# Kernel optimization log

Hardware: AMD Instinct MI355X
Metric: run time of the kernel (lower is better)

## Reference

```python
import jax, jax.numpy as jnp
import numpy as np

T, B, N_IN, N_H = 1024, 64, 128, 512

def setup_inputs() -> dict:
    key = jax.random.key(0)
    k1, k2, k3 = jax.random.split(key, 3)
    x = jax.random.normal(k1, (T, B, N_IN), dtype=jnp.float32)
    h0 = jax.random.normal(k2, (B, N_H), dtype=jnp.float32)
    # scale recurrent weights ~ 1/sqrt(fan_in) so tanh does not saturate
    w_rec = jax.random.normal(k3, (N_H, N_H + N_IN + 1), dtype=jnp.float32) * (1.0 / np.sqrt(N_H + N_IN + 1))
    return {"x": x, "h0": h0, "w_rec": w_rec}

def reference(x, h0, w_rec):
    # Elman RNN: h_t = tanh(w_rec @ [h_{t-1}; x_t; 1])
    # x: [T, B, n_in], h0: [B, n_h], w_rec: [n_h, n_h + n_in + 1]
    n_h = h0.shape[-1]
    w_h = w_rec[:, :n_h]            # [n_h, n_h]
    w_x = w_rec[:, n_h:-1]          # [n_h, n_in]
    b = w_rec[:, -1]                # [n_h]
    # precompute input projections for all steps: [T, B, n_h]
    xin = jnp.einsum('tbi,hi->tbh', x, w_x) + b
    def step(h, u):
        h_new = jnp.tanh(jnp.einsum('bk,hk->bh', h, w_h) + u)
        return h_new, h_new
    _, hs = jax.lax.scan(step, h0, xin)
    return hs  # [T, B, n_h]
```

## Files before the change

### kernel.cpp

```cpp
#include <hip/hip_runtime.h>


typedef _Float16 h2 __attribute__((ext_vector_type(2)));

#define T_STEPS 1024
#define B_SZ    64
#define NIN     128
#define NH      512
#define WCOLS   641

__device__ __forceinline__ float fdot2_(h2 a, h2 b, float c) {
#if __has_builtin(__builtin_amdgcn_fdot2)
    return __builtin_amdgcn_fdot2(a, b, c, false);
#else
    return c + (float)a.x * (float)b.x + (float)a.y * (float)b.y;
#endif
}

__device__ __forceinline__ float dot8(uint4 wu, uint4 hu, float acc) {
    union { uint4 u; h2 h[4]; } w, hv;
    w.u = wu; hv.u = hu;
    acc = fdot2_(w.h[0], hv.h[0], acc);
    acc = fdot2_(w.h[1], hv.h[1], acc);
    acc = fdot2_(w.h[2], hv.h[2], acc);
    acc = fdot2_(w.h[3], hv.h[3], acc);
    return acc;
}

__device__ __forceinline__ float fast_tanh(float x) {
    float z = x * 2.8853900817779268f;
#if __has_builtin(__builtin_amdgcn_exp2f)
    float e = __builtin_amdgcn_exp2f(z);
#else
    float e = exp2f(z);
#endif
#if __has_builtin(__builtin_amdgcn_rcpf)
    return 1.f - 2.f * __builtin_amdgcn_rcpf(e + 1.f);
#else
    return 1.f - 2.f / (e + 1.f);
#endif
}

template<int CTRL>
__device__ __forceinline__ float dpp_add(float x) {
    int y = __builtin_amdgcn_update_dpp(0, __builtin_bit_cast(int, x),
                                        CTRL, 0xF, 0xF, true);
    return x + __builtin_bit_cast(float, y);
}

__global__ void prep_kernel(const float* __restrict__ w_rec,
                            float* __restrict__ wxT,
                            float* __restrict__ bias,
                            uint4* __restrict__ Whpk) {
    int g = blockIdx.x * 256 + threadIdx.x;
    if (g < NIN * NH) {
        int i = g >> 9, h = g & (NH - 1);
        wxT[g] = w_rec[h * WCOLS + NH + i];
    } else if (g < NIN * NH + 64 * NH) {
        int m   = g - NIN * NH;
        int c   = m >> 9, tid = m & 511;
        int w   = tid >> 6, lane = tid & 63;
        int rl  = lane >> 3, kl = lane & 7;
        int i   = c & 7, j = c >> 3;
        int row = w * 64 + i * 8 + rl;
        int kg  = kl * 8 + j;
        union { uint4 u; _Float16 f[8]; } pk;
#pragma unroll
        for (int e = 0; e < 8; ++e)
            pk.f[e] = (_Float16)w_rec[row * WCOLS + kg * 8 + e];
        Whpk[c * 512 + tid] = pk.u;
    } else if (g < NIN * NH + 64 * NH + NH) {
        int h = g - (NIN * NH + 64 * NH);
        bias[h] = w_rec[h * WCOLS + NH + NIN];
    }
}

__global__ __launch_bounds__(256) void xin_gemm(const float* __restrict__ x,
                                                const float* __restrict__ wxT,
                                                const float* __restrict__ bias,
                                                float* __restrict__ out) {
    __shared__ float4 xl[128 * 8];
    __shared__ float4 wl[32 * 32];
    __shared__ float  bs[128];
    const int tid = threadIdx.x;
    const int tb0 = blockIdx.x * 128;
    const int hc0 = blockIdx.y * 128;
    if (tid < 128) bs[tid] = bias[hc0 + tid];
    const int tx = tid & 15, ty = tid >> 4;

    float acc[8][8];
#pragma unroll
    for (int r = 0; r < 8; ++r)
#pragma unroll
        for (int c = 0; c < 8; ++c) acc[r][c] = 0.f;

    for (int kc = 0; kc < 4; ++kc) {
        __syncthreads();
#pragma unroll
        for (int l = 0; l < 4; ++l) {
            int idx = tid + 256 * l;
            int row = idx >> 3, c4 = idx & 7;
            xl[idx] = *(const float4*)(x + (long)(tb0 + row) * NIN + kc * 32 + c4 * 4);
        }
#pragma unroll
        for (int l = 0; l < 4; ++l) {
            int idx = tid + 256 * l;
            int ii = idx >> 5, c4 = idx & 31;
            wl[idx] = *(const float4*)(wxT + (kc * 32 + ii) * NH + hc0 + c4 * 4);
        }
        __syncthreads();
#pragma unroll
        for (int i4 = 0; i4 < 8; ++i4) {
            float4 xv[8];
#pragma unroll
            for (int rr = 0; rr < 8; ++rr) xv[rr] = xl[(ty * 8 + rr) * 8 + i4];
#pragma unroll
            for (int j = 0; j < 4; ++j) {
                float4 w0 = wl[(i4 * 4 + j) * 32 + tx * 2];
                float4 w1 = wl[(i4 * 4 + j) * 32 + tx * 2 + 1];
#pragma unroll
                for (int rr = 0; rr < 8; ++rr) {
                    float xs = (j == 0) ? xv[rr].x : (j == 1) ? xv[rr].y
                             : (j == 2) ? xv[rr].z : xv[rr].w;
                    acc[rr][0] += xs * w0.x; acc[rr][1] += xs * w0.y;
                    acc[rr][2] += xs * w0.z; acc[rr][3] += xs * w0.w;
                    acc[rr][4] += xs * w1.x; acc[rr][5] += xs * w1.y;
                    acc[rr][6] += xs * w1.z; acc[rr][7] += xs * w1.w;
                }
            }
        }
    }
#pragma unroll
    for (int rr = 0; rr < 8; ++rr) {
        long row = tb0 + ty * 8 + rr;
        float4 o0, o1;
        o0.x = acc[rr][0] + bs[tx * 8 + 0]; o0.y = acc[rr][1] + bs[tx * 8 + 1];
        o0.z = acc[rr][2] + bs[tx * 8 + 2]; o0.w = acc[rr][3] + bs[tx * 8 + 3];
        o1.x = acc[rr][4] + bs[tx * 8 + 4]; o1.y = acc[rr][5] + bs[tx * 8 + 5];
        o1.z = acc[rr][6] + bs[tx * 8 + 6]; o1.w = acc[rr][7] + bs[tx * 8 + 7];
        *(float4*)(out + row * NH + hc0 + tx * 8)     = o0;
        *(float4*)(out + row * NH + hc0 + tx * 8 + 4) = o1;
    }
}

__global__ __launch_bounds__(512, 2) void rnn_scan(float* __restrict__ out,
                                                   const float* __restrict__ h0,
                                                   const uint4* __restrict__ Whpk) {
    __shared__ uint4 Wl[16 * 512];
    __shared__ uint4 hh[2][72];

    const int tid  = threadIdx.x;
    const int b    = blockIdx.x;
    const int w    = tid >> 6;
    const int lane = tid & 63;
    const int rl   = lane >> 3;
    const int kl   = lane & 7;

#pragma unroll
    for (int c = 0; c < 16; ++c) Wl[c * 512 + tid] = Whpk[(32 + c) * 512 + tid];

    uint4 Wreg[32];
#pragma unroll
    for (int c = 0; c < 32; ++c) Wreg[c] = Whpk[c * 512 + tid];

    {
        int g = tid >> 3, e = tid & 7;
        _Float16* p = (_Float16*)&hh[0][g + (g >> 3)];
        p[e] = (_Float16)h0[b * NH + tid];
    }
    __syncthreads();

    const int own = w * 64 + kl * 8 + rl;
    float* pu = out + (long)b * NH + own;
    float u_cur = *pu;

    for (int t = 0; t < T_STEPS; ++t) {
        const uint4* hc = hh[t & 1];
        uint4 bufA[4], bufB[4];

#pragma unroll
        for (int i = 0; i < 4; ++i) bufA[i] = Whpk[(48 + i) * 512 + tid];
        long stride = (t + 1 < T_STEPS) ? (long)B_SZ * NH : 0;
        float u_nxt = pu[stride];
#pragma unroll
        for (int i = 0; i < 4; ++i) bufB[i] = Whpk[(52 + i) * 512 + tid];

        uint4 hs[8];
#pragma unroll
        for (int j = 0; j < 8; ++j) hs[j] = hc[9 * kl + j];

        float acc[8];
#pragma unroll
        for (int i = 0; i < 8; ++i) acc[i] = 0.f;

#pragma unroll
        for (int j = 0; j < 4; ++j)
#pragma unroll
            for (int i = 0; i < 8; ++i)
                acc[i] = dot8(Wreg[j * 8 + i], hs[j], acc[i]);

#pragma unroll
        for (int i = 0; i < 4; ++i) acc[i] = dot8(bufA[i], hs[6], acc[i]);
#pragma unroll
        for (int i = 0; i < 4; ++i) bufA[i] = Whpk[(56 + i) * 512 + tid];

#pragma unroll
        for (int i = 0; i < 4; ++i) acc[4 + i] = dot8(bufB[i], hs[6], acc[4 + i]);
#pragma unroll
        for (int i = 0; i < 4; ++i) bufB[i] = Whpk[(60 + i) * 512 + tid];

#pragma unroll
        for (int j = 0; j < 2; ++j)
#pragma unroll
            for (int i = 0; i < 8; ++i)
                acc[i] = dot8(Wl[(j * 8 + i) * 512 + tid], hs[4 + j], acc[i]);

#pragma unroll
        for (int i = 0; i < 4; ++i) acc[i] = dot8(bufA[i], hs[7], acc[i]);
#pragma unroll
        for (int i = 0; i < 4; ++i) acc[4 + i] = dot8(bufB[i], hs[7], acc[4 + i]);

#pragma unroll
        for (int i = 0; i < 8; ++i) {
            acc[i] = dpp_add<0xB1>(acc[i]);
            acc[i] = dpp_add<0x4E>(acc[i]);
            acc[i] = dpp_add<0x141>(acc[i]);
        }

        float a01 = (kl & 1) ? acc[1] : acc[0];
        float a23 = (kl & 1) ? acc[3] : acc[2];
        float a45 = (kl & 1) ? acc[5] : acc[4];
        float a67 = (kl & 1) ? acc[7] : acc[6];
        float b03 = (kl & 2) ? a23 : a01;
        float b47 = (kl & 2) ? a67 : a45;
        float sel = (kl & 4) ? b47 : b03;

        float hnew = fast_tanh(sel + u_cur);
        u_cur = u_nxt;
        *pu = hnew;
        pu += B_SZ * NH;

        {
            _Float16* p = (_Float16*)&hh[(t + 1) & 1][9 * w + kl];
            p[rl] = (_Float16)hnew;
        }
        __syncthreads();
    }
}

extern "C" void kernel_launch(void* const* d_in, const int* in_sizes, int n_in,
                              void* d_out, int out_size, void* d_ws, size_t ws_size,
                              hipStream_t stream) {
    const float* x     = (const float*)d_in[0];
    const float* h0    = (const float*)d_in[1];
    const float* w_rec = (const float*)d_in[2];
    float* out = (float*)d_out;

    float* wxT  = (float*)d_ws;
    float* bias = wxT + NIN * NH;
    uint4* Whpk = (uint4*)((char*)d_ws + (NIN * NH + NH) * sizeof(float));

    prep_kernel<<<387, 256, 0, stream>>>(w_rec, wxT, bias, Whpk);

    dim3 gA(T_STEPS * B_SZ / 128, NH / 128);
    xin_gemm<<<gA, 256, 0, stream>>>(x, wxT, bias, out);

    rnn_scan<<<B_SZ, NH, 0, stream>>>(out, h0, Whpk);
}
```

Baseline: 1.785 ms.

## Split each batch row's recurrence across four workgroups with flag-tagged global exchange

Each batch row's recurrent matvec is now split across four workgroups, each owning 128 hidden rows. That lets the whole weight slice live in registers, with no LDS or streamed global weight loads per step. Newly computed hidden values are packed with a step tag and written to a global exchange buffer that bypasses the nearby cache level. An extra wave per workgroup spins until all tags match, then gathers the full hidden state into LDS. The kernel is launched cooperatively so all 256 workgroups are co-resident. The exchange buffer reuses the workspace that held the transposed input weights, and the per-step cross-CU round trip adds latency that must stay below the compute it saves.

```diff
diff --git a/kernel.cpp b/kernel.cpp
--- a/kernel.cpp
+++ b/kernel.cpp
@@ -48,6 +48,21 @@
     return x + __builtin_bit_cast(float, y);
 }
 
+__device__ __forceinline__ uint4 ld128_sc1(const void* p) {
+    uint4 r;
+    asm volatile("global_load_dwordx4 %0, %1, off sc1"
+                 : "=v"(r) : "v"(p) : "memory");
+    return r;
+}
+__device__ __forceinline__ void st64_sc1(void* p, unsigned long long v) {
+    asm volatile("global_store_dwordx2 %0, %1, off sc1"
+                 :: "v"(p), "v"(v) : "memory");
+}
+__device__ __forceinline__ void wait_vm0() {
+    asm volatile("s_waitcnt vmcnt(0)" ::: "memory");
+    __builtin_amdgcn_sched_barrier(0);
+}
+
 __global__ void prep_kernel(const float* __restrict__ w_rec,
                             float* __restrict__ wxT,
                             float* __restrict__ bias,
@@ -58,17 +73,18 @@
         wxT[g] = w_rec[h * WCOLS + NH + i];
     } else if (g < NIN * NH + 64 * NH) {
         int m   = g - NIN * NH;
-        int c   = m >> 9, tid = m & 511;
+        int cg  = m >> 9, tid = m & 511;
+        int q   = cg >> 4, c = cg & 15;
+        int i   = c & 1, j = c >> 1;
         int w   = tid >> 6, lane = tid & 63;
         int rl  = lane >> 3, kl = lane & 7;
-        int i   = c & 7, j = c >> 3;
-        int row = w * 64 + i * 8 + rl;
+        int row = q * 128 + w * 16 + rl * 2 + i;
         int kg  = kl * 8 + j;
         union { uint4 u; _Float16 f[8]; } pk;
 #pragma unroll
         for (int e = 0; e < 8; ++e)
             pk.f[e] = (_Float16)w_rec[row * WCOLS + kg * 8 + e];
-        Whpk[c * 512 + tid] = pk.u;
+        Whpk[cg * 512 + tid] = pk.u;
     } else if (g < NIN * NH + 64 * NH + NH) {
         int h = g - (NIN * NH + 64 * NH);
         bias[h] = w_rec[h * WCOLS + NH + NIN];
@@ -143,107 +159,90 @@
     }
 }
 
-__global__ __launch_bounds__(512, 2) void rnn_scan(float* __restrict__ out,
+__global__ __launch_bounds__(576, 2) void rnn_scan(float* __restrict__ out,
                                                    const float* __restrict__ h0,
-                                                   const uint4* __restrict__ Whpk) {
-    __shared__ uint4 Wl[16 * 512];
+                                                   const uint4* __restrict__ Whpk,
+                                                   unsigned long long* __restrict__ hx2) {
+    __shared__ int  lds_pad[20484];
     __shared__ uint4 hh[2][72];
 
-    const int tid  = threadIdx.x;
-    const int b    = blockIdx.x;
-    const int w    = tid >> 6;
-    const int lane = tid & 63;
-    const int rl   = lane >> 3;
-    const int kl   = lane & 7;
-
-#pragma unroll
-    for (int c = 0; c < 16; ++c) Wl[c * 512 + tid] = Whpk[(32 + c) * 512 + tid];
-
-    uint4 Wreg[32];
-#pragma unroll
-    for (int c = 0; c < 32; ++c) Wreg[c] = Whpk[c * 512 + tid];
-
-    {
+    const int tid = threadIdx.x, wg = blockIdx.x;
+    const int b = wg & 63, q = wg >> 6;
+    const int w = tid >> 6, lane = tid & 63, rl = lane >> 3, kl = lane & 7;
+    ((volatile int*)lds_pad)[tid] = 0;
+
+    uint4 Wreg[16];
+    if (tid < 512) {
+#pragma unroll
+        for (int c = 0; c < 16; ++c) Wreg[c] = Whpk[(q * 16 + c) * 512 + tid];
+    }
+
+    if (tid < 512) {
         int g = tid >> 3, e = tid & 7;
         _Float16* p = (_Float16*)&hh[0][g + (g >> 3)];
         p[e] = (_Float16)h0[b * NH + tid];
     }
+
+    const int rowpair = q * 128 + w * 16 + rl * 2;
+    const int rpo = q * 64 + w * 8 + rl;
+    float* pu = out + (long)b * NH + rowpair;
+    float2 u_cur = make_float2(0.f, 0.f);
+    if (tid < 512 && kl == 0) u_cur = *(const float2*)pu;
+    unsigned long long* const hxb = hx2 + b * 256;
+
     __syncthreads();
 
-    const int own = w * 64 + kl * 8 + rl;
-    float* pu = out + (long)b * NH + own;
-    float u_cur = *pu;
-
     for (int t = 0; t < T_STEPS; ++t) {
-        const uint4* hc = hh[t & 1];
-        uint4 bufA[4], bufB[4];
-
-#pragma unroll
-        for (int i = 0; i < 4; ++i) bufA[i] = Whpk[(48 + i) * 512 + tid];
-        long stride = (t + 1 < T_STEPS) ? (long)B_SZ * NH : 0;
-        float u_nxt = pu[stride];
-#pragma unroll
-        for (int i = 0; i < 4; ++i) bufB[i] = Whpk[(52 + i) * 512 + tid];
-
-        uint4 hs[8];
-#pragma unroll
-        for (int j = 0; j < 8; ++j) hs[j] = hc[9 * kl + j];
-
-        float acc[8];
-#pragma unroll
-        for (int i = 0; i < 8; ++i) acc[i] = 0.f;
-
-#pragma unroll
-        for (int j = 0; j < 4; ++j)
-#pragma unroll
-            for (int i = 0; i < 8; ++i)
-                acc[i] = dot8(Wreg[j * 8 + i], hs[j], acc[i]);
-
-#pragma unroll
-        for (int i = 0; i < 4; ++i) acc[i] = dot8(bufA[i], hs[6], acc[i]);
-#pragma unroll
-        for (int i = 0; i < 4; ++i) bufA[i] = Whpk[(56 + i) * 512 + tid];
-
-#pragma unroll
-        for (int i = 0; i < 4; ++i) acc[4 + i] = dot8(bufB[i], hs[6], acc[4 + i]);
-#pragma unroll
-        for (int i = 0; i < 4; ++i) bufB[i] = Whpk[(60 + i) * 512 + tid];
-
-#pragma unroll
-        for (int j = 0; j < 2; ++j)
-#pragma unroll
-            for (int i = 0; i < 8; ++i)
-                acc[i] = dot8(Wl[(j * 8 + i) * 512 + tid], hs[4 + j], acc[i]);
-
-#pragma unroll
-        for (int i = 0; i < 4; ++i) acc[i] = dot8(bufA[i], hs[7], acc[i]);
-#pragma unroll
-        for (int i = 0; i < 4; ++i) acc[4 + i] = dot8(bufB[i], hs[7], acc[4 + i]);
-
-#pragma unroll
-        for (int i = 0; i < 8; ++i) {
-            acc[i] = dpp_add<0xB1>(acc[i]);
-            acc[i] = dpp_add<0x4E>(acc[i]);
-            acc[i] = dpp_add<0x141>(acc[i]);
-        }
-
-        float a01 = (kl & 1) ? acc[1] : acc[0];
-        float a23 = (kl & 1) ? acc[3] : acc[2];
-        float a45 = (kl & 1) ? acc[5] : acc[4];
-        float a67 = (kl & 1) ? acc[7] : acc[6];
-        float b03 = (kl & 2) ? a23 : a01;
-        float b47 = (kl & 2) ? a67 : a45;
-        float sel = (kl & 4) ? b47 : b03;
-
-        float hnew = fast_tanh(sel + u_cur);
-        u_cur = u_nxt;
-        *pu = hnew;
-        pu += B_SZ * NH;
-
-        {
-            _Float16* p = (_Float16*)&hh[(t + 1) & 1][9 * w + kl];
-            p[rl] = (_Float16)hnew;
-        }
+        if (tid < 512) {
+            const uint4* hc = hh[t & 1];
+            uint4 hsv[8];
+#pragma unroll
+            for (int j = 0; j < 8; ++j) hsv[j] = hc[9 * kl + j];
+
+            float a00 = 0.f, a01 = 0.f, a10 = 0.f, a11 = 0.f;
+#pragma unroll
+            for (int j = 0; j < 8; j += 2) {
+                a00 = dot8(Wreg[j * 2 + 0], hsv[j],     a00);
+                a10 = dot8(Wreg[j * 2 + 1], hsv[j],     a10);
+                a01 = dot8(Wreg[j * 2 + 2], hsv[j + 1], a01);
+                a11 = dot8(Wreg[j * 2 + 3], hsv[j + 1], a11);
+            }
+            float acc0 = a00 + a01, acc1 = a10 + a11;
+            acc0 = dpp_add<0xB1>(acc0); acc0 = dpp_add<0x4E>(acc0); acc0 = dpp_add<0x141>(acc0);
+            acc1 = dpp_add<0xB1>(acc1); acc1 = dpp_add<0x4E>(acc1); acc1 = dpp_add<0x141>(acc1);
+
+            if (kl == 0) {
+                long stride = (t + 1 < T_STEPS) ? (long)B_SZ * NH : 0;
+                float2 u_nxt = *(const float2*)(pu + stride);
+                float hv0 = fast_tanh(acc0 + u_cur.x);
+                float hv1 = fast_tanh(acc1 + u_cur.y);
+                *(float2*)pu = make_float2(hv0, hv1);
+                h2 hp; hp.x = (_Float16)hv0; hp.y = (_Float16)hv1;
+                unsigned long long pk =
+                    ((unsigned long long)(unsigned)(t + 1) << 32)
+                    | (unsigned long long)__builtin_bit_cast(unsigned int, hp);
+                st64_sc1(hxb + ((t + 1) & 1) * 16384 + rpo, pk);
+                u_cur = u_nxt;
+            }
+            pu += (long)B_SZ * NH;
+        } else if (t + 1 < T_STEPS) {
+            const int L = tid - 512;
+            const unsigned want = (unsigned)(t + 1);
+            const char* src = (const char*)(hxb + ((t + 1) & 1) * 16384) + L * 32;
+            uint4 va = ld128_sc1(src);
+            uint4 vb = ld128_sc1(src + 16);
+            wait_vm0();
+            for (;;) {
+                int ok = (va.y == want) & (va.w == want) &
+                         (vb.y == want) & (vb.w == want);
+                if (__all(ok)) break;
+                if (va.y != want || va.w != want) va = ld128_sc1(src);
+                if (vb.y != want || vb.w != want) vb = ld128_sc1(src + 16);
+                wait_vm0();
+            }
+            hh[(t + 1) & 1][L + (L >> 3)] = make_uint4(va.x, va.z, vb.x, vb.z);
+        }
+        if (t + 1 == T_STEPS) break;
         __syncthreads();
     }
 }
@@ -259,11 +258,16 @@
     float* wxT  = (float*)d_ws;
     float* bias = wxT + NIN * NH;
     uint4* Whpk = (uint4*)((char*)d_ws + (NIN * NH + NH) * sizeof(float));
-
-    prep_kernel<<<387, 256, 0, stream>>>(w_rec, wxT, bias, Whpk);
+    unsigned long long* hx2 = (unsigned long long*)d_ws;
+
+    prep_kernel<<<386, 256, 0, stream>>>(w_rec, wxT, bias, Whpk);
 
     dim3 gA(T_STEPS * B_SZ / 128, NH / 128);
     xin_gemm<<<gA, 256, 0, stream>>>(x, wxT, bias, out);
 
-    rnn_scan<<<B_SZ, NH, 0, stream>>>(out, h0, Whpk);
-}
+    void* args[] = { (void*)&out, (void*)&h0, (void*)&Whpk, (void*)&hx2 };
+    if (hipLaunchCooperativeKernel((const void*)rnn_scan, dim3(256), dim3(576),
+                                   args, 0, stream) != hipSuccess) {
+        rnn_scan<<<256, 576, 0, stream>>>(out, h0, Whpk, hx2);
+    }
+}
```

Result: slower. 2.387 ms (+33.8%).

## Keep 48 weight chunks in registers via inline asm loads, drop per-step global refetch

Applied to the files above, without the earlier changes.

Before, each step refetched 16 weight chunks from global or L2 into small rotating buffers. Now 48 chunks are loaded once into named registers through inline-asm global loads, so the compiler cannot rematerialize or spill them. The remaining 16 chunks stay in shared memory, and the final step skips its barrier. This removes per-step global weight traffic from the serial recurrence, but with launch bounds (512,2) it needs about 192 VGPRs just for weights, which risks spills or lower occupancy.

```diff
diff --git a/kernel.cpp b/kernel.cpp
--- a/kernel.cpp
+++ b/kernel.cpp
@@ -149,24 +149,27 @@
     __shared__ uint4 Wl[16 * 512];
     __shared__ uint4 hh[2][72];
 
-    const int tid  = threadIdx.x;
-    const int b    = blockIdx.x;
-    const int w    = tid >> 6;
-    const int lane = tid & 63;
-    const int rl   = lane >> 3;
-    const int kl   = lane & 7;
-
-#pragma unroll
-    for (int c = 0; c < 16; ++c) Wl[c * 512 + tid] = Whpk[(32 + c) * 512 + tid];
-
-    uint4 Wreg[32];
-#pragma unroll
-    for (int c = 0; c < 32; ++c) Wreg[c] = Whpk[c * 512 + tid];
+    const int tid = threadIdx.x, b = blockIdx.x;
+    const int w = tid >> 6, lane = tid & 63, rl = lane >> 3, kl = lane & 7;
+
+#pragma unroll
+    for (int c = 0; c < 16; ++c) Wl[c * 512 + tid] = Whpk[(48 + c) * 512 + tid];
+
+#define LOADW(n) uint4 W##n; { const uint4* p_ = Whpk + (n) * 512 + tid;      \
+    asm volatile("global_load_dwordx4 %0, %1, off" : "=v"(W##n) : "v"(p_)); }
+    LOADW(0)  LOADW(1)  LOADW(2)  LOADW(3)  LOADW(4)  LOADW(5)  LOADW(6)  LOADW(7)
+    LOADW(8)  LOADW(9)  LOADW(10) LOADW(11) LOADW(12) LOADW(13) LOADW(14) LOADW(15)
+    LOADW(16) LOADW(17) LOADW(18) LOADW(19) LOADW(20) LOADW(21) LOADW(22) LOADW(23)
+    LOADW(24) LOADW(25) LOADW(26) LOADW(27) LOADW(28) LOADW(29) LOADW(30) LOADW(31)
+    LOADW(32) LOADW(33) LOADW(34) LOADW(35) LOADW(36) LOADW(37) LOADW(38) LOADW(39)
+    LOADW(40) LOADW(41) LOADW(42) LOADW(43) LOADW(44) LOADW(45) LOADW(46) LOADW(47)
+#undef LOADW
+    asm volatile("s_waitcnt vmcnt(0)" ::: "memory");
+    __builtin_amdgcn_sched_barrier(0);
 
     {
         int g = tid >> 3, e = tid & 7;
-        _Float16* p = (_Float16*)&hh[0][g + (g >> 3)];
-        p[e] = (_Float16)h0[b * NH + tid];
+        ((_Float16*)&hh[0][g + (g >> 3)])[e] = (_Float16)h0[b * NH + tid];
     }
     __syncthreads();
 
@@ -176,14 +179,9 @@
 
     for (int t = 0; t < T_STEPS; ++t) {
         const uint4* hc = hh[t & 1];
-        uint4 bufA[4], bufB[4];
-
-#pragma unroll
-        for (int i = 0; i < 4; ++i) bufA[i] = Whpk[(48 + i) * 512 + tid];
+
         long stride = (t + 1 < T_STEPS) ? (long)B_SZ * NH : 0;
         float u_nxt = pu[stride];
-#pragma unroll
-        for (int i = 0; i < 4; ++i) bufB[i] = Whpk[(52 + i) * 512 + tid];
 
         uint4 hs[8];
 #pragma unroll
@@ -193,32 +191,18 @@
 #pragma unroll
         for (int i = 0; i < 8; ++i) acc[i] = 0.f;
 
-#pragma unroll
-        for (int j = 0; j < 4; ++j)
-#pragma unroll
-            for (int i = 0; i < 8; ++i)
-                acc[i] = dot8(Wreg[j * 8 + i], hs[j], acc[i]);
-
-#pragma unroll
-        for (int i = 0; i < 4; ++i) acc[i] = dot8(bufA[i], hs[6], acc[i]);
-#pragma unroll
-        for (int i = 0; i < 4; ++i) bufA[i] = Whpk[(56 + i) * 512 + tid];
-
-#pragma unroll
-        for (int i = 0; i < 4; ++i) acc[4 + i] = dot8(bufB[i], hs[6], acc[4 + i]);
-#pragma unroll
-        for (int i = 0; i < 4; ++i) bufB[i] = Whpk[(60 + i) * 512 + tid];
-
-#pragma unroll
-        for (int j = 0; j < 2; ++j)
-#pragma unroll
-            for (int i = 0; i < 8; ++i)
-                acc[i] = dot8(Wl[(j * 8 + i) * 512 + tid], hs[4 + j], acc[i]);
-
-#pragma unroll
-        for (int i = 0; i < 4; ++i) acc[i] = dot8(bufA[i], hs[7], acc[i]);
-#pragma unroll
-        for (int i = 0; i < 4; ++i) acc[4 + i] = dot8(bufB[i], hs[7], acc[4 + i]);
+#define DOTW(n) acc[(n) & 7] = dot8(W##n, hs[(n) >> 3], acc[(n) & 7]);
+        DOTW(0)  DOTW(1)  DOTW(2)  DOTW(3)  DOTW(4)  DOTW(5)  DOTW(6)  DOTW(7)
+        DOTW(8)  DOTW(9)  DOTW(10) DOTW(11) DOTW(12) DOTW(13) DOTW(14) DOTW(15)
+        DOTW(16) DOTW(17) DOTW(18) DOTW(19) DOTW(20) DOTW(21) DOTW(22) DOTW(23)
+        DOTW(24) DOTW(25) DOTW(26) DOTW(27) DOTW(28) DOTW(29) DOTW(30) DOTW(31)
+        DOTW(32) DOTW(33) DOTW(34) DOTW(35) DOTW(36) DOTW(37) DOTW(38) DOTW(39)
+        DOTW(40) DOTW(41) DOTW(42) DOTW(43) DOTW(44) DOTW(45) DOTW(46) DOTW(47)
+#undef DOTW
+
+#pragma unroll
+        for (int c = 0; c < 16; ++c)
+            acc[c & 7] = dot8(Wl[c * 512 + tid], hs[6 + (c >> 3)], acc[c & 7]);
 
 #pragma unroll
         for (int i = 0; i < 8; ++i) {
@@ -238,12 +222,10 @@
         float hnew = fast_tanh(sel + u_cur);
         u_cur = u_nxt;
         *pu = hnew;
-        pu += B_SZ * NH;
-
-        {
-            _Float16* p = (_Float16*)&hh[(t + 1) & 1][9 * w + kl];
-            p[rl] = (_Float16)hnew;
-        }
+        ((_Float16*)&hh[(t + 1) & 1][9 * w + kl])[rl] = (_Float16)hnew;
+        pu += (long)B_SZ * NH;
+
+        if (t + 1 == T_STEPS) break;
         __syncthreads();
     }
 }
```

New measurement: 1.688 ms. 5.5% less time.
